# Performance work log

Hardware: AMD Instinct MI355X
Metric: run time of the kernel (lower is better)

The kernel has to match this reference:

```python
import jax, jax.numpy as jnp
import numpy as np

N = 8192          # nodes per type (MiRNA, Disease, T)
E = 500000        # edges per relation
FEAT = 256
HID = 64
OUT = 128
ITEM = 8192
SIZE = 4096
LEFT = 0
# relation order: 0:MvsD(M->D) 1:DvsM(D->M) 2:MvsT(M->T) 3:TvsM(T->M) 4:TvsD(T->D) 5:DvsT(D->T)


def graph_conv(x, W, b, src, dst, n_src, n_dst):
    outdeg = jax.ops.segment_sum(jnp.ones(src.shape, x.dtype), src, num_segments=n_src)
    xs = (x * (jnp.maximum(outdeg, 1.0) ** -0.5)[:, None]) @ W
    agg = jax.ops.segment_sum(xs[src], dst, num_segments=n_dst)
    indeg = jax.ops.segment_sum(jnp.ones(dst.shape, x.dtype), dst, num_segments=n_dst)
    return agg * (jnp.maximum(indeg, 1.0) ** -0.5)[:, None] + b


def hetero_layer(hM, hD, hT, W, b, edges):
    srcs = [hM, hD, hM, hT, hT, hD]
    outs = [graph_conv(srcs[i], W[i], b[i], edges[i, 0], edges[i, 1], N, N) for i in range(6)]
    # aggregate='sum' per destination type
    newM = outs[1] + outs[3]
    newD = outs[0] + outs[4]
    newT = outs[2] + outs[5]
    return newM, newD, newT


def setup_inputs() -> dict:
    key = jax.random.key(0)
    ks = jax.random.split(key, 24)

    def glorot(k, shape):
        lim = np.sqrt(6.0 / (shape[-2] + shape[-1]))
        return jax.random.uniform(k, shape, jnp.float32, -lim, lim)

    inp = {
        'hM': jax.random.normal(ks[0], (N, FEAT), jnp.float32),
        'hD': jax.random.normal(ks[1], (N, FEAT), jnp.float32),
        'hT': jax.random.normal(ks[2], (N, FEAT), jnp.float32),
        'W1': glorot(ks[3], (6, FEAT, HID)), 'b1': jnp.zeros((6, HID), jnp.float32),
        'W2': glorot(ks[4], (6, HID, HID)), 'b2': jnp.zeros((6, HID), jnp.float32),
        'W3': glorot(ks[5], (6, HID, OUT)), 'b3': jnp.zeros((6, OUT), jnp.float32),
        'Adj': (jax.random.uniform(ks[6], (SIZE, ITEM)) < 0.05).astype(jnp.float32),
        'f1_w': glorot(ks[7], (ITEM + OUT, 256)), 'f1_b': jnp.zeros((256,), jnp.float32),
        'f2_w': glorot(ks[8], (256, 512)), 'f2_b': jnp.zeros((512,), jnp.float32),
        'f3_w': glorot(ks[9], (512, 1024)), 'f3_b': jnp.zeros((1024,), jnp.float32),
        'f4_w': glorot(ks[10], (1024, ITEM)), 'f4_b': jnp.zeros((ITEM,), jnp.float32),
        'edges': jax.random.randint(ks[11], (6, 2, E), 0, N, dtype=jnp.int32),
        'size': SIZE,
        'leftIndex': LEFT,
    }
    return inp


def reference(hM, hD, hT, W1, b1, W2, b2, W3, b3, Adj,
              f1_w, f1_b, f2_w, f2_b, f3_w, f3_b, f4_w, f4_b,
              edges, size, leftIndex):
    hM1, hD1, hT1 = hetero_layer(hM, hD, hT, W1, b1, edges)
    hM2, hD2, hT2 = hetero_layer(hM1, hD1, hT1, W2, b2, edges)
    hM3, hD3, hT3 = hetero_layer(hM2, hD2, hT2, W3, b3, edges)
    # torch.nn.functional.normalize(p=1, dim=1)
    mirna = hM3 / jnp.maximum(jnp.sum(jnp.abs(hM3), axis=1, keepdims=True), 1e-12)
    fake_embeding = mirna[leftIndex:leftIndex + size]
    M = jnp.concatenate([Adj, fake_embeding], axis=1)
    x = jax.nn.relu(M @ f1_w + f1_b)
    x = jax.nn.relu(x @ f2_w + f2_b)
    x = jax.nn.relu(x @ f3_w + f3_b)
    x = jax.nn.sigmoid(x @ f4_w + f4_b)
    return fake_embeding, x
```

## Files before the change

kernel.cpp:

```cpp
#include <hip/hip_runtime.h>
#include <hip/hip_bf16.h>
#include <cstdint>
#include <cstddef>
#include <type_traits>

#define NN 8192
#define NTYPE 6
#define BPT 32

typedef __attribute__((ext_vector_type(8))) short bf16x8;
typedef __attribute__((ext_vector_type(4))) float f32x4;
typedef __attribute__((ext_vector_type(4))) unsigned short u16x4;
typedef __attribute__((ext_vector_type(8))) unsigned short u16x8;

#define GLOAD16(g, l)                                                        \
  __builtin_amdgcn_global_load_lds(                                          \
      (const __attribute__((address_space(1))) void*)(g),                    \
      (__attribute__((address_space(3))) void*)(l), 16, 0, 0)

static __device__ __forceinline__ unsigned short f2bf(float f) {
  union { float f; unsigned u; } x; x.f = f;
  unsigned u = x.u + 0x7fffu + ((x.u >> 16) & 1u);
  return (unsigned short)(u >> 16);
}
static __device__ __forceinline__ float bf2f(unsigned short u) {
  union { unsigned u32; float f; } x; x.u32 = (unsigned)u << 16; return x.f;
}

__global__ __launch_bounds__(256) void hist_degree(
    const int* __restrict__ edges, int* __restrict__ partial, int E) {
  const int b = blockIdx.x, t = blockIdx.y, role = blockIdx.z;
  __shared__ int h[NN];
  for (int i = threadIdx.x; i < NN; i += 256) h[i] = 0;
  __syncthreads();
  const int* ids = edges + ((size_t)t * 2 + role) * E;
  int ch = (E + BPT - 1) / BPT;
  int beg = b * ch, end = (beg + ch < E) ? beg + ch : E;
  for (int i = beg + threadIdx.x; i < end; i += 256)
    atomicAdd(&h[__builtin_nontemporal_load(ids + i)], 1);
  __syncthreads();
  int* dst = partial + ((size_t)((role * NTYPE + t) * BPT + b)) * NN;
  for (int i = threadIdx.x; i < NN; i += 256) dst[i] = h[i];
}

__global__ __launch_bounds__(256) void reduce_deg(
    const int* __restrict__ partial, float* __restrict__ inv_out,
    float* __restrict__ inv_in, int* __restrict__ incnt) {
  int i = blockIdx.x * 256 + threadIdx.x;
  if (i >= NTYPE * NN) return;
  int t = i >> 13, n = i & (NN - 1);
  const int* ps = partial + ((size_t)(t * BPT)) * NN + n;
  const int* pd = partial + ((size_t)((NTYPE + t) * BPT)) * NN + n;
  int so = 0, sd = 0;
#pragma unroll 8
  for (int b = 0; b < BPT; ++b) { so += ps[(size_t)b * NN]; sd += pd[(size_t)b * NN]; }
  inv_out[i] = rsqrtf(fmaxf((float)so, 1.0f));
  inv_in[i]  = rsqrtf(fmaxf((float)sd, 1.0f));
  incnt[i]   = sd;
}

__global__ void scan_rows(const int* __restrict__ incnt, int* __restrict__ row_start) {
  int t = blockIdx.x;
  int i = threadIdx.x;
  const int* c = incnt + t * NN;
  int v[8], s = 0;
#pragma unroll
  for (int j = 0; j < 8; ++j) { v[j] = c[i * 8 + j]; s += v[j]; }
  __shared__ int p[1024];
  p[i] = s;
  __syncthreads();
  for (int d = 1; d < 1024; d <<= 1) {
    int x = (i >= d) ? p[i - d] : 0;
    __syncthreads();
    p[i] += x;
    __syncthreads();
  }
  int run = p[i] - s;
  int* rs = row_start + t * (NN + 1);
#pragma unroll
  for (int j = 0; j < 8; ++j) { rs[i * 8 + j] = run; run += v[j]; }
  if (i == 1023) rs[NN] = run;
}

__global__ __launch_bounds__(256) void slice_offsets(
    const int* __restrict__ partial, const int* __restrict__ row_start,
    int* __restrict__ soff) {
  int i = blockIdx.x * 256 + threadIdx.x;
  if (i >= NTYPE * NN) return;
  int t = i >> 13, d = i & (NN - 1);
  const int* pd = partial + ((size_t)((NTYPE + t) * BPT)) * NN + d;
  int run = row_start[t * (NN + 1) + d];
  int* o = soff + ((size_t)t * BPT) * NN + d;
#pragma unroll 8
  for (int s = 0; s < BPT; ++s) { o[(size_t)s * NN] = run; run += pd[(size_t)s * NN]; }
}

__global__ __launch_bounds__(256) void scatter_v2(
    const int* __restrict__ edges, const int* __restrict__ soff,
    int* __restrict__ csr, int E) {
  int t = blockIdx.x;
  if (t >= NTYPE) return;
  int s = blockIdx.y;
  __shared__ int cur[NN];
  const int* o = soff + ((size_t)(t * BPT + s)) * NN;
  for (int i = threadIdx.x; i < NN; i += 256) cur[i] = o[i];
  __syncthreads();
  int ch = (E + BPT - 1) / BPT;
  int beg = s * ch, end = (beg + ch < E) ? beg + ch : E;
  const int* eb = edges + (size_t)t * 2 * E;
  int* out = csr + (size_t)t * E;
  for (int i = beg + threadIdx.x; i < end; i += 256) {
    int src = __builtin_nontemporal_load(eb + i);
    int dst = __builtin_nontemporal_load(eb + E + i);
    int pos = atomicAdd(&cur[dst], 1);
    out[pos] = src;
  }
}

__global__ __launch_bounds__(256) void gemm64xs(
    const float* __restrict__ p0, const float* __restrict__ p1,
    const float* __restrict__ p2, int lda,
    const float* __restrict__ WL, const float* __restrict__ inv_out,
    unsigned short* __restrict__ xs6, int F, int H, int tpack) {
  const int t = (tpack >> (4 * blockIdx.z)) & 15;
  const int srcc[6] = {0, 1, 0, 2, 2, 1};
  const float* A = (srcc[t] == 0) ? p0 : (srcc[t] == 1) ? p1 : p2;
  const float* B = WL + (size_t)t * F * H;
  const float* rscale = inv_out + t * NN;
  unsigned short* out = xs6 + (size_t)t * NN * H;

  __shared__ float As[16][68];
  __shared__ float Bs[16][68];
  int tid = threadIdx.x;
  int n0 = blockIdx.x * 64, m0 = blockIdx.y * 64;
  int ar = tid >> 2, ac = (tid & 3) * 4;
  int br = tid >> 4, bc = (tid & 15) * 4;
  int tx = tid & 15, ty = tid >> 4;
  float acc[4][4] = {};
  for (int k0 = 0; k0 < F; k0 += 16) {
    float4 av = *(const float4*)(A + (size_t)(m0 + ar) * lda + k0 + ac);
    As[ac + 0][ar] = av.x; As[ac + 1][ar] = av.y;
    As[ac + 2][ar] = av.z; As[ac + 3][ar] = av.w;
    *(float4*)&Bs[br][bc] = *(const float4*)(B + (size_t)(k0 + br) * H + n0 + bc);
    __syncthreads();
#pragma unroll
    for (int kk = 0; kk < 16; ++kk) {
      float4 a = *(const float4*)&As[kk][ty * 4];
      float4 b = *(const float4*)&Bs[kk][tx * 4];
      float aa[4] = {a.x, a.y, a.z, a.w};
      float bb[4] = {b.x, b.y, b.z, b.w};
#pragma unroll
      for (int i = 0; i < 4; ++i)
#pragma unroll
        for (int j = 0; j < 4; ++j) acc[i][j] += aa[i] * bb[j];
    }
    __syncthreads();
  }
#pragma unroll
  for (int i = 0; i < 4; ++i) {
    int r = m0 + ty * 4 + i;
    float sc = rscale[r];
    union { unsigned short us[4]; short4 v; } pk;
#pragma unroll
    for (int j = 0; j < 4; ++j) pk.us[j] = f2bf(acc[i][j] * sc);
    *(short4*)&out[(size_t)r * H + n0 + tx * 4] = pk.v;
  }
}

template <int H>
__global__ __launch_bounds__(256) void aggregate3(
    const unsigned short* __restrict__ xs6, const int* __restrict__ csr,
    const int* __restrict__ row_start, const float* __restrict__ inv_in,
    const float* __restrict__ bL, float* __restrict__ feat_out, int E, int cpack) {
  constexpr int VE = H / 16;
  const int c = (cpack >> (8 * blockIdx.y)) & 0xff;
  const int taT[3] = {1, 0, 2}, tbT[3] = {3, 4, 5};
  int wave = threadIdx.x >> 6, lane = threadIdx.x & 63;
  int slot = lane >> 4, colg = lane & 15;
  int d = blockIdx.x * 4 + wave;

  float out[VE];
#pragma unroll
  for (int v = 0; v < VE; ++v) out[v] = 0.f;

#pragma unroll
  for (int half = 0; half < 2; ++half) {
    int t = half ? tbT[c] : taT[c];
    const unsigned short* xs = xs6 + (size_t)t * NN * H;
    const int* cs = csr + (size_t)t * E;
    const int* rs = row_start + t * (NN + 1);
    int b = rs[d], e = rs[d + 1];
    float a[VE];
#pragma unroll
    for (int v = 0; v < VE; ++v) a[v] = 0.f;
    for (int j0 = b; j0 < e; j0 += 64) {
      int myj = j0 + lane;
      int idxv = (myj < e) ? cs[myj] : 0;
      int cnt = e - j0; if (cnt > 64) cnt = 64;
      int g = 0;
      for (; (g + 1) * 4 <= cnt; ++g) {
        int is = __shfl(idxv, g * 4 + slot);
        const unsigned short* xr = xs + (size_t)is * H + colg * VE;
        if constexpr (VE == 4) {
          u16x4 x = *(const u16x4*)xr;
#pragma unroll
          for (int v = 0; v < 4; ++v) a[v] += bf2f(x[v]);
        } else {
          u16x8 x = *(const u16x8*)xr;
#pragma unroll
          for (int v = 0; v < 8; ++v) a[v] += bf2f(x[v]);
        }
      }
      int done = g * 4;
      if (done < cnt) {
        int gi = done + slot;
        int is = __shfl(idxv, gi < cnt ? gi : 0);
        float wt = (gi < cnt) ? 1.0f : 0.0f;
        const unsigned short* xr = xs + (size_t)is * H + colg * VE;
        if constexpr (VE == 4) {
          u16x4 x = *(const u16x4*)xr;
#pragma unroll
          for (int v = 0; v < 4; ++v) a[v] += wt * bf2f(x[v]);
        } else {
          u16x8 x = *(const u16x8*)xr;
#pragma unroll
          for (int v = 0; v < 8; ++v) a[v] += wt * bf2f(x[v]);
        }
      }
    }
    float sc = inv_in[t * NN + d];
#pragma unroll
    for (int v = 0; v < VE; ++v) out[v] += a[v] * sc;
  }
#pragma unroll
  for (int v = 0; v < VE; ++v) {
    out[v] += __shfl_xor(out[v], 16);
    out[v] += __shfl_xor(out[v], 32);
  }
  if (lane < 16) {
    int ta = taT[c], tb = tbT[c];
    float* o = feat_out + (size_t)c * NN * 128 + (size_t)d * H + colg * VE;
    const float* ba = bL + ta * H + colg * VE;
    const float* bb = bL + tb * H + colg * VE;
    float4 w0 = make_float4(out[0] + ba[0] + bb[0], out[1] + ba[1] + bb[1],
                            out[2] + ba[2] + bb[2], out[3] + ba[3] + bb[3]);
    *(float4*)o = w0;
    if constexpr (VE == 8) {
      float4 w1 = make_float4(out[4] + ba[4] + bb[4], out[5] + ba[5] + bb[5],
                              out[6] + ba[6] + bb[6], out[7] + ba[7] + bb[7]);
      *(float4*)(o + 4) = w1;
    }
  }
}

__global__ __launch_bounds__(256) void l1norm_fake(
    const float* __restrict__ hM3, const int* __restrict__ leftIndex,
    float* __restrict__ fake) {
  int wave = threadIdx.x >> 6, lane = threadIdx.x & 63;
  int r = blockIdx.x * 4 + wave;
  int row = leftIndex[0] + r;
  const float* x = hM3 + (size_t)row * 128;
  float a = x[lane], b = x[64 + lane];
  float s = fabsf(a) + fabsf(b);
#pragma unroll
  for (int d = 1; d < 64; d <<= 1) s += __shfl_xor(s, d);
  float inv = 1.0f / fmaxf(s, 1e-12f);
  fake[(size_t)r * 128 + lane]      = a * inv;
  fake[(size_t)r * 128 + 64 + lane] = b * inv;
}

__global__ __launch_bounds__(256) void castT4(
    const float* __restrict__ i0, unsigned short* __restrict__ o0,
    const float* __restrict__ i1, unsigned short* __restrict__ o1,
    const float* __restrict__ i2, unsigned short* __restrict__ o2,
    const float* __restrict__ i3, unsigned short* __restrict__ o3) {
  const int nb0 = (8320 / 32) * (256 / 32);
  const int nb1 = (256 / 32) * (512 / 32);
  const int nb2 = (512 / 32) * (1024 / 32);
  int b = blockIdx.x;
  const float* in; unsigned short* out; int K, N;
  if (b < nb0) { in = i0; out = o0; K = 8320; N = 256; }
  else if ((b -= nb0) < nb1) { in = i1; out = o1; K = 256; N = 512; }
  else if ((b -= nb1) < nb2) { in = i2; out = o2; K = 512; N = 1024; }
  else { b -= nb2; in = i3; out = o3; K = 1024; N = 8192; }
  int nx = N / 32;
  int n0 = (b % nx) * 32, k0 = (b / nx) * 32;

  __shared__ float t[32][33];
  int tx = threadIdx.x & 31, ty = threadIdx.x >> 5;
#pragma unroll
  for (int i = 0; i < 32; i += 8)
    t[ty + i][tx] = in[(size_t)(k0 + ty + i) * N + n0 + tx];
  __syncthreads();
#pragma unroll
  for (int i = 0; i < 32; i += 8)
    out[(size_t)(n0 + ty + i) * K + k0 + tx] = f2bf(t[tx][ty + i]);
}

template <int ASRC, int ACT>
__global__ __launch_bounds__(256) void mfma_gemm(
    const unsigned short* __restrict__ Abf, int lda,
    const float* __restrict__ A1, const float* __restrict__ A2,
    int K1, int lda1, int lda2,
    const unsigned short* __restrict__ Bt, int ldb,
    const float* __restrict__ bias,
    void* __restrict__ outp, int ldo, int K, int kchunk, int pstride) {
  __shared__ unsigned short As[128 * 32];
  __shared__ unsigned short Bs[128 * 32];
  const int tid = threadIdx.x;
  const int n0 = blockIdx.x * 128, m0 = blockIdx.y * 128;
  const int wave = tid >> 6, lane = tid & 63;
  const int lq = lane >> 4, lr = lane & 15;
  const int wm = wave >> 1, wn = wave & 1;
  const int kbeg = blockIdx.z * kchunk;
  const int kend = (kbeg + kchunk < K) ? (kbeg + kchunk) : K;

  f32x4 acc[4][4] = {};

  const int G0 = tid, G1 = tid + 256;
  const int r0 = G0 >> 2, c0 = ((G0 & 3) - (r0 >> 1)) & 3;
  const int r1 = G1 >> 2, c1 = ((G1 & 3) - (r1 >> 1)) & 3;
  const int wbase0 = (tid & ~63) * 8;
  const int wbase1 = wbase0 + 256 * 8;

  for (int k0 = kbeg; k0 < kend; k0 += 32) {
    GLOAD16(Bt + (size_t)(n0 + r0) * ldb + k0 + c0 * 8, &Bs[wbase0]);
    GLOAD16(Bt + (size_t)(n0 + r1) * ldb + k0 + c1 * 8, &Bs[wbase1]);
    if (ASRC == 0) {
      GLOAD16(Abf + (size_t)(m0 + r0) * lda + k0 + c0 * 8, &As[wbase0]);
      GLOAD16(Abf + (size_t)(m0 + r1) * lda + k0 + c1 * 8, &As[wbase1]);
    } else {
#pragma unroll
      for (int q = 0; q < 2; ++q) {
        int r = q ? r1 : r0, c = q ? c1 : c0, G = q ? G1 : G0;
        int kk = k0 + c * 8;
        const float* src = (kk < K1) ? (A1 + (size_t)(m0 + r) * lda1 + kk)
                                     : (A2 + (size_t)(m0 + r) * lda2 + (kk - K1));
        float4 u = *(const float4*)src;
        float4 v = *(const float4*)(src + 4);
        union { unsigned short us[8]; bf16x8 v8; } pk;
        pk.us[0] = f2bf(u.x); pk.us[1] = f2bf(u.y);
        pk.us[2] = f2bf(u.z); pk.us[3] = f2bf(u.w);
        pk.us[4] = f2bf(v.x); pk.us[5] = f2bf(v.y);
        pk.us[6] = f2bf(v.z); pk.us[7] = f2bf(v.w);
        *(bf16x8*)&As[G * 8] = pk.v8;
      }
    }
    __syncthreads();

    const int cs = (lq + (lr >> 1)) & 3;
    const int rA = wm * 64 + lr, rB = wn * 64 + lr;
    bf16x8 af[4], bfr[4];
#pragma unroll
    for (int m = 0; m < 4; ++m)
      af[m] = *(const bf16x8*)&As[(((rA + m * 16) << 2) + cs) << 3];
#pragma unroll
    for (int n = 0; n < 4; ++n)
      bfr[n] = *(const bf16x8*)&Bs[(((rB + n * 16) << 2) + cs) << 3];
#pragma unroll
    for (int m = 0; m < 4; ++m)
#pragma unroll
      for (int n = 0; n < 4; ++n)
        acc[m][n] = __builtin_amdgcn_mfma_f32_16x16x32_bf16(af[m], bfr[n], acc[m][n], 0, 0, 0);
    __syncthreads();
  }

  const int rowb = m0 + wm * 64 + lq * 4;
  const int colb = n0 + wn * 64 + lr;
  float* pout = (ACT == 0) ? ((float*)outp + (size_t)blockIdx.z * pstride) : (float*)outp;
#pragma unroll
  for (int n = 0; n < 4; ++n) {
    int c = colb + n * 16;
    float bv = (ACT == 0) ? 0.0f : bias[c];
#pragma unroll
    for (int m = 0; m < 4; ++m) {
      int r = rowb + m * 16;
#pragma unroll
      for (int j = 0; j < 4; ++j) {
        float v = acc[m][n][j] + bv;
        if (ACT == 0) {
          pout[(size_t)(r + j) * ldo + c] = v;
        } else {
          v = fmaxf(v, 0.0f);
          ((unsigned short*)outp)[(size_t)(r + j) * ldo + c] = f2bf(v);
        }
      }
    }
  }
}

__global__ __launch_bounds__(512, 1) void gemm256sig(
    const unsigned short* __restrict__ A, int lda,
    const unsigned short* __restrict__ Bt, int ldb,
    const float* __restrict__ bias,
    float* __restrict__ out, int ldo) {
  __shared__ unsigned short sA[2][8192];
  __shared__ unsigned short sB[2][8192];
  const int tid = threadIdx.x;
  const int wave = tid >> 6, lane = tid & 63;
  const int lq = lane >> 4, lr = lane & 15;
  const int wm = wave >> 2, wn = wave & 3;
  const int bid = blockIdx.x;
  const int xcd = bid & 7, kb = bid >> 3;
  const int n0 = (xcd * 4 + (kb & 3)) * 256;
  const int m0 = (kb >> 2) * 256;

  f32x4 acc[8][4] = {};

  const int ra0 = tid >> 2, ca0 = tid & 3;
  const int ra1 = ra0 + 128, ca1 = ca0;
  const int sl0 = (ra0 << 2) + ((ca0 + (ra0 >> 1)) & 3);
  const int sl1 = (ra1 << 2) + ((ca1 + (ra1 >> 1)) & 3);

  u16x8 gA0, gA1, gB0, gB1;
  auto g_issue = [&](int h) {
    int kk = h * 32;
    gA0 = *(const u16x8*)(A  + (size_t)(m0 + ra0) * lda + kk + ca0 * 8);
    gA1 = *(const u16x8*)(A  + (size_t)(m0 + ra1) * lda + kk + ca1 * 8);
    gB0 = *(const u16x8*)(Bt + (size_t)(n0 + ra0) * ldb + kk + ca0 * 8);
    gB1 = *(const u16x8*)(Bt + (size_t)(n0 + ra1) * ldb + kk + ca1 * 8);
  };
  auto l_write = [&](int buf) {
    *(u16x8*)&sA[buf][sl0 * 8] = gA0;
    *(u16x8*)&sA[buf][sl1 * 8] = gA1;
    *(u16x8*)&sB[buf][sl0 * 8] = gB0;
    *(u16x8*)&sB[buf][sl1 * 8] = gB1;
  };

  g_issue(0);
  l_write(0);
  g_issue(1);
  __syncthreads();

#pragma unroll 1
  for (int h = 0; h < 32; ++h) {
    const int cur = h & 1, nxt = cur ^ 1;
    const unsigned short* pa = &sA[cur][0];
    const unsigned short* pb = &sB[cur][0];
    bf16x8 afv[8], bfv[4];
#pragma unroll
    for (int n = 0; n < 4; ++n) {
      int r = wn * 64 + n * 16 + lr;
      bfv[n] = *(const bf16x8*)&pb[(size_t)(((r << 2) + ((lq + (r >> 1)) & 3)) << 3)];
    }
#pragma unroll
    for (int m = 0; m < 8; ++m) {
      int r = wm * 128 + m * 16 + lr;
      afv[m] = *(const bf16x8*)&pa[(size_t)(((r << 2) + ((lq + (r >> 1)) & 3)) << 3)];
    }
    if (h + 1 < 32) l_write(nxt);
    if (h + 2 < 32) g_issue(h + 2);
    __builtin_amdgcn_s_setprio(1);
#pragma unroll
    for (int m = 0; m < 8; ++m)
#pragma unroll
      for (int n = 0; n < 4; ++n)
        acc[m][n] = __builtin_amdgcn_mfma_f32_16x16x32_bf16(afv[m], bfv[n], acc[m][n], 0, 0, 0);
    __builtin_amdgcn_s_setprio(0);
    __syncthreads();
  }

  float* lw = (wave < 4) ? ((float*)&sA[0][0] + wave * 2048)
                         : ((float*)&sB[0][0] + (wave - 4) * 2048);
  const int rowb = m0 + wm * 128;
  const int colb = n0 + wn * 64;
  float bv[4];
#pragma unroll
  for (int n = 0; n < 4; ++n) bv[n] = bias[colb + n * 16 + lr];
#pragma unroll
  for (int m = 0; m < 8; ++m) {
#pragma unroll
    for (int n = 0; n < 4; ++n)
#pragma unroll
      for (int j = 0; j < 4; ++j) {
        float v = acc[m][n][j] + bv[n];
        v = 1.0f / (1.0f + __expf(-v));
        lw[(lq * 4 + j) * 68 + n * 16 + lr] = v;
      }
    asm volatile("s_waitcnt lgkmcnt(0)" ::: "memory");
#pragma unroll
    for (int i = 0; i < 4; ++i) {
      int chunk = i * 64 + lane;
      int rr = chunk >> 4, cg = chunk & 15;
      f32x4 val = *(f32x4*)&lw[rr * 68 + cg * 4];
      __builtin_nontemporal_store(
          val, (f32x4*)(out + (size_t)(rowb + m * 16 + rr) * ldo + colb + cg * 4));
    }
    asm volatile("s_waitcnt lgkmcnt(0)" ::: "memory");
  }
}

__global__ __launch_bounds__(256) void reduceK(
    const float* __restrict__ part, const float* __restrict__ bias,
    unsigned short* __restrict__ out, int total, int N, int nsplit, int pstride) {
  int idx = blockIdx.x * 256 + threadIdx.x;
  int base = idx * 4;
  if (base >= total) return;
  float4 s = *(const float4*)(part + base);
  for (int z = 1; z < nsplit; ++z) {
    float4 p = *(const float4*)(part + (size_t)z * pstride + base);
    s.x += p.x; s.y += p.y; s.z += p.z; s.w += p.w;
  }
  float4 bv = *(const float4*)(bias + (base & (N - 1)));
  union { unsigned short us[4]; short4 v; } pk;
  pk.us[0] = f2bf(fmaxf(s.x + bv.x, 0.0f));
  pk.us[1] = f2bf(fmaxf(s.y + bv.y, 0.0f));
  pk.us[2] = f2bf(fmaxf(s.z + bv.z, 0.0f));
  pk.us[3] = f2bf(fmaxf(s.w + bv.w, 0.0f));
  *(short4*)&out[base] = pk.v;
}

extern "C" void kernel_launch(void* const* d_in, const int* in_sizes, int n_in,
                              void* d_out, int out_size, void* d_ws, size_t ws_size,
                              hipStream_t stream) {
  const float* hM  = (const float*)d_in[0];
  const float* hD  = (const float*)d_in[1];
  const float* hT  = (const float*)d_in[2];
  const float* W1  = (const float*)d_in[3];
  const float* b1  = (const float*)d_in[4];
  const float* W2  = (const float*)d_in[5];
  const float* b2  = (const float*)d_in[6];
  const float* W3  = (const float*)d_in[7];
  const float* b3  = (const float*)d_in[8];
  const float* Adj = (const float*)d_in[9];
  const float* f1w = (const float*)d_in[10];
  const float* f1b = (const float*)d_in[11];
  const float* f2w = (const float*)d_in[12];
  const float* f2b = (const float*)d_in[13];
  const float* f3w = (const float*)d_in[14];
  const float* f3b = (const float*)d_in[15];
  const float* f4w = (const float*)d_in[16];
  const float* f4b = (const float*)d_in[17];
  const int* edges = (const int*)d_in[18];
  const int* leftIndex = (const int*)d_in[20];
  const int E = in_sizes[18] / 12;
  (void)ws_size; (void)n_in; (void)out_size;

  char* w = (char*)d_ws;
  size_t off = 0;
  auto alloc = [&](size_t bytes) {
    void* p = w + off;
    off = (off + bytes + 255) & ~(size_t)255;
    return p;
  };
  int*   row_start = (int*)  alloc((size_t)NTYPE * (NN + 1) * 4);
  int*   incnt     = (int*)  alloc((size_t)NTYPE * NN * 4);
  float* inv_out   = (float*)alloc((size_t)NTYPE * NN * 4);
  float* inv_in    = (float*)alloc((size_t)NTYPE * NN * 4);
  float* featA     = (float*)alloc((size_t)3 * NN * 128 * 4);
  size_t ubase = off;
  int*            csr   = (int*)           alloc((size_t)NTYPE * E * 4);
  unsigned short* xs6   = (unsigned short*)alloc((size_t)NTYPE * NN * 128 * 2);
  float*          featB = (float*)         alloc((size_t)3 * NN * 128 * 4);
  int* deg_part = (int*)csr;
  int* soff     = (int*)featB;
  size_t moff = ubase;
  auto malloc2 = [&](size_t bytes) {
    void* p = w + moff;
    moff = (moff + bytes + 255) & ~(size_t)255;
    return p;
  };
  unsigned short* w1t = (unsigned short*)malloc2((size_t)256 * 8320 * 2);
  unsigned short* w2t = (unsigned short*)malloc2((size_t)512 * 256 * 2);
  unsigned short* w3t = (unsigned short*)malloc2((size_t)1024 * 512 * 2);
  unsigned short* w4t = (unsigned short*)malloc2((size_t)8192 * 1024 * 2);
  unsigned short* x1b = (unsigned short*)malloc2((size_t)4096 * 256 * 2);
  unsigned short* x2b = (unsigned short*)malloc2((size_t)4096 * 512 * 2);
  unsigned short* x3b = (unsigned short*)malloc2((size_t)4096 * 1024 * 2);
  float*          x1p = (float*)malloc2((size_t)8 * 4096 * 256 * 4);

  hist_degree<<<dim3(BPT, NTYPE, 2), 256, 0, stream>>>(edges, deg_part, E);
  reduce_deg<<<(NTYPE * NN + 255) / 256, 256, 0, stream>>>(deg_part, inv_out, inv_in, incnt);
  scan_rows<<<NTYPE, 1024, 0, stream>>>(incnt, row_start);
  slice_offsets<<<(NTYPE * NN + 255) / 256, 256, 0, stream>>>(deg_part, row_start, soff);
  scatter_v2<<<dim3(8, BPT), 256, 0, stream>>>(edges, soff, csr, E);

  const size_t comp = (size_t)NN * 128;
  gemm64xs<<<dim3(1, NN / 64, 6), 256, 0, stream>>>(
      hM, hD, hT, 256, W1, inv_out, xs6, 256, 64, 0x543210);
  aggregate3<64><<<dim3(NN / 4, 3), 256, 0, stream>>>(
      xs6, csr, row_start, inv_in, b1, featA, E, 0x020100);
  gemm64xs<<<dim3(1, NN / 64, 4), 256, 0, stream>>>(
      featA, featA + comp, featA + 2 * comp, 64, W2, inv_out, xs6, 64, 64, 0x5420);
  aggregate3<64><<<dim3(NN / 4, 2), 256, 0, stream>>>(
      xs6, csr, row_start, inv_in, b2, featB, E, 0x0201);
  gemm64xs<<<dim3(2, NN / 64, 2), 256, 0, stream>>>(
      featB, featB + comp, featB + 2 * comp, 64, W3, inv_out, xs6, 64, 128, 0x31);
  aggregate3<128><<<dim3(NN / 4, 1), 256, 0, stream>>>(
      xs6, csr, row_start, inv_in, b3, featA, E, 0x00);

  float* fake = (float*)d_out;
  float* outx = (float*)d_out + (size_t)4096 * 128;
  l1norm_fake<<<4096 / 4, 256, 0, stream>>>(featA, leftIndex, fake);

  const int ncast = (8320 / 32) * (256 / 32) + (256 / 32) * (512 / 32) +
                    (512 / 32) * (1024 / 32) + (8192 / 32) * (1024 / 32);
  castT4<<<ncast, 256, 0, stream>>>(f1w, w1t, f2w, w2t, f3w, w3t, f4w, w4t);

  mfma_gemm<1, 0><<<dim3(256 / 128, 4096 / 128, 8), 256, 0, stream>>>(
      nullptr, 0, Adj, fake, 8192, 8192, 128, w1t, 8320, nullptr,
      x1p, 256, 8320, 1056, 4096 * 256);
  reduceK<<<(4096 * 256 / 4 + 255) / 256, 256, 0, stream>>>(
      x1p, f1b, x1b, 4096 * 256, 256, 8, 4096 * 256);
  mfma_gemm<0, 1><<<dim3(512 / 128, 4096 / 128), 256, 0, stream>>>(
      x1b, 256, nullptr, nullptr, 0, 0, 0, w2t, 256, f2b, x2b, 512, 256, 256, 0);
  mfma_gemm<0, 1><<<dim3(1024 / 128, 4096 / 128), 256, 0, stream>>>(
      x2b, 512, nullptr, nullptr, 0, 0, 0, w3t, 512, f3b, x3b, 1024, 512, 512, 0);
  gemm256sig<<<512, 512, 0, stream>>>(x3b, 1024, w4t, 1024, f4b, outx, 8192);
}
```

Before: 416.0 us.

## Fuse degree/scan/offset kernels and aggregate only the needed output rows

Merges the degree reduction, row scan and slice-offset kernels into one kernel with one 1024-thread block per relation. The last-layer aggregation now computes only the 4096 destination rows starting at leftIndex that feed the MLP, instead of all 8192. The fp32 A-operand loads in the MFMA GEMM become nontemporal loads. The fused kernel removes two launches and the incnt buffer, but it runs on only 6 blocks, so the 12 MB partial-histogram read loses parallelism.

```diff
diff --git a/kernel.cpp b/kernel.cpp
--- a/kernel.cpp
+++ b/kernel.cpp
@@ -43,34 +43,34 @@
   for (int i = threadIdx.x; i < NN; i += 256) dst[i] = h[i];
 }
 
-__global__ __launch_bounds__(256) void reduce_deg(
+__global__ __launch_bounds__(1024) void build_offsets(
     const int* __restrict__ partial, float* __restrict__ inv_out,
-    float* __restrict__ inv_in, int* __restrict__ incnt) {
-  int i = blockIdx.x * 256 + threadIdx.x;
-  if (i >= NTYPE * NN) return;
-  int t = i >> 13, n = i & (NN - 1);
-  const int* ps = partial + ((size_t)(t * BPT)) * NN + n;
-  const int* pd = partial + ((size_t)((NTYPE + t) * BPT)) * NN + n;
-  int so = 0, sd = 0;
+    float* __restrict__ inv_in, int* __restrict__ row_start,
+    int* __restrict__ soff) {
+  const int t = blockIdx.x, i = threadIdx.x;
+  const int* ps = partial + (size_t)(t * BPT) * NN;
+  const int* pd = partial + (size_t)((NTYPE + t) * BPT) * NN;
+  for (int d = i; d < NN; d += 1024) {
+    int so = 0;
 #pragma unroll 8
-  for (int b = 0; b < BPT; ++b) { so += ps[(size_t)b * NN]; sd += pd[(size_t)b * NN]; }
-  inv_out[i] = rsqrtf(fmaxf((float)so, 1.0f));
-  inv_in[i]  = rsqrtf(fmaxf((float)sd, 1.0f));
-  incnt[i]   = sd;
-}
-
-__global__ void scan_rows(const int* __restrict__ incnt, int* __restrict__ row_start) {
-  int t = blockIdx.x;
-  int i = threadIdx.x;
-  const int* c = incnt + t * NN;
+    for (int b = 0; b < BPT; ++b) so += ps[(size_t)b * NN + d];
+    inv_out[t * NN + d] = rsqrtf(fmaxf((float)so, 1.0f));
+  }
   int v[8], s = 0;
 #pragma unroll
-  for (int j = 0; j < 8; ++j) { v[j] = c[i * 8 + j]; s += v[j]; }
+  for (int j = 0; j < 8; ++j) {
+    int d = i * 8 + j;
+    int sd = 0;
+#pragma unroll 8
+    for (int b = 0; b < BPT; ++b) sd += pd[(size_t)b * NN + d];
+    v[j] = sd; s += sd;
+    inv_in[t * NN + d] = rsqrtf(fmaxf((float)sd, 1.0f));
+  }
   __shared__ int p[1024];
   p[i] = s;
   __syncthreads();
-  for (int d = 1; d < 1024; d <<= 1) {
-    int x = (i >= d) ? p[i - d] : 0;
+  for (int dd = 1; dd < 1024; dd <<= 1) {
+    int x = (i >= dd) ? p[i - dd] : 0;
     __syncthreads();
     p[i] += x;
     __syncthreads();
@@ -80,19 +80,16 @@
 #pragma unroll
   for (int j = 0; j < 8; ++j) { rs[i * 8 + j] = run; run += v[j]; }
   if (i == 1023) rs[NN] = run;
-}
-
-__global__ __launch_bounds__(256) void slice_offsets(
-    const int* __restrict__ partial, const int* __restrict__ row_start,
-    int* __restrict__ soff) {
-  int i = blockIdx.x * 256 + threadIdx.x;
-  if (i >= NTYPE * NN) return;
-  int t = i >> 13, d = i & (NN - 1);
-  const int* pd = partial + ((size_t)((NTYPE + t) * BPT)) * NN + d;
-  int run = row_start[t * (NN + 1) + d];
-  int* o = soff + ((size_t)t * BPT) * NN + d;
+  __syncthreads();
+  int* o = soff + (size_t)t * BPT * NN;
+  for (int d = i; d < NN; d += 1024) {
+    int r2 = rs[d];
 #pragma unroll 8
-  for (int s = 0; s < BPT; ++s) { o[(size_t)s * NN] = run; run += pd[(size_t)s * NN]; }
+    for (int sl = 0; sl < BPT; ++sl) {
+      o[(size_t)sl * NN + d] = r2;
+      r2 += pd[(size_t)sl * NN + d];
+    }
+  }
 }
 
 __global__ __launch_bounds__(256) void scatter_v2(
@@ -171,13 +168,15 @@
 __global__ __launch_bounds__(256) void aggregate3(
     const unsigned short* __restrict__ xs6, const int* __restrict__ csr,
     const int* __restrict__ row_start, const float* __restrict__ inv_in,
-    const float* __restrict__ bL, float* __restrict__ feat_out, int E, int cpack) {
+    const float* __restrict__ bL, float* __restrict__ feat_out, int E, int cpack,
+    const int* __restrict__ dbase) {
   constexpr int VE = H / 16;
   const int c = (cpack >> (8 * blockIdx.y)) & 0xff;
   const int taT[3] = {1, 0, 2}, tbT[3] = {3, 4, 5};
   int wave = threadIdx.x >> 6, lane = threadIdx.x & 63;
   int slot = lane >> 4, colg = lane & 15;
   int d = blockIdx.x * 4 + wave;
+  if (dbase) d += dbase[0];
 
   float out[VE];
 #pragma unroll
@@ -336,13 +335,13 @@
         int kk = k0 + c * 8;
         const float* src = (kk < K1) ? (A1 + (size_t)(m0 + r) * lda1 + kk)
                                      : (A2 + (size_t)(m0 + r) * lda2 + (kk - K1));
-        float4 u = *(const float4*)src;
-        float4 v = *(const float4*)(src + 4);
+        f32x4 u = __builtin_nontemporal_load((const f32x4*)src);
+        f32x4 vv = __builtin_nontemporal_load((const f32x4*)(src + 4));
         union { unsigned short us[8]; bf16x8 v8; } pk;
-        pk.us[0] = f2bf(u.x); pk.us[1] = f2bf(u.y);
-        pk.us[2] = f2bf(u.z); pk.us[3] = f2bf(u.w);
-        pk.us[4] = f2bf(v.x); pk.us[5] = f2bf(v.y);
-        pk.us[6] = f2bf(v.z); pk.us[7] = f2bf(v.w);
+        pk.us[0] = f2bf(u[0]); pk.us[1] = f2bf(u[1]);
+        pk.us[2] = f2bf(u[2]); pk.us[3] = f2bf(u[3]);
+        pk.us[4] = f2bf(vv[0]); pk.us[5] = f2bf(vv[1]);
+        pk.us[6] = f2bf(vv[2]); pk.us[7] = f2bf(vv[3]);
         *(bf16x8*)&As[G * 8] = pk.v8;
       }
     }
@@ -544,7 +543,6 @@
     return p;
   };
   int*   row_start = (int*)  alloc((size_t)NTYPE * (NN + 1) * 4);
-  int*   incnt     = (int*)  alloc((size_t)NTYPE * NN * 4);
   float* inv_out   = (float*)alloc((size_t)NTYPE * NN * 4);
   float* inv_in    = (float*)alloc((size_t)NTYPE * NN * 4);
   float* featA     = (float*)alloc((size_t)3 * NN * 128 * 4);
@@ -570,24 +568,22 @@
   float*          x1p = (float*)malloc2((size_t)8 * 4096 * 256 * 4);
 
   hist_degree<<<dim3(BPT, NTYPE, 2), 256, 0, stream>>>(edges, deg_part, E);
-  reduce_deg<<<(NTYPE * NN + 255) / 256, 256, 0, stream>>>(deg_part, inv_out, inv_in, incnt);
-  scan_rows<<<NTYPE, 1024, 0, stream>>>(incnt, row_start);
-  slice_offsets<<<(NTYPE * NN + 255) / 256, 256, 0, stream>>>(deg_part, row_start, soff);
+  build_offsets<<<NTYPE, 1024, 0, stream>>>(deg_part, inv_out, inv_in, row_start, soff);
   scatter_v2<<<dim3(8, BPT), 256, 0, stream>>>(edges, soff, csr, E);
 
   const size_t comp = (size_t)NN * 128;
   gemm64xs<<<dim3(1, NN / 64, 6), 256, 0, stream>>>(
       hM, hD, hT, 256, W1, inv_out, xs6, 256, 64, 0x543210);
   aggregate3<64><<<dim3(NN / 4, 3), 256, 0, stream>>>(
-      xs6, csr, row_start, inv_in, b1, featA, E, 0x020100);
+      xs6, csr, row_start, inv_in, b1, featA, E, 0x020100, nullptr);
   gemm64xs<<<dim3(1, NN / 64, 4), 256, 0, stream>>>(
       featA, featA + comp, featA + 2 * comp, 64, W2, inv_out, xs6, 64, 64, 0x5420);
   aggregate3<64><<<dim3(NN / 4, 2), 256, 0, stream>>>(
-      xs6, csr, row_start, inv_in, b2, featB, E, 0x0201);
+      xs6, csr, row_start, inv_in, b2, featB, E, 0x0201, nullptr);
   gemm64xs<<<dim3(2, NN / 64, 2), 256, 0, stream>>>(
       featB, featB + comp, featB + 2 * comp, 64, W3, inv_out, xs6, 64, 128, 0x31);
-  aggregate3<128><<<dim3(NN / 4, 1), 256, 0, stream>>>(
-      xs6, csr, row_start, inv_in, b3, featA, E, 0x00);
+  aggregate3<128><<<dim3(4096 / 4, 1), 256, 0, stream>>>(
+      xs6, csr, row_start, inv_in, b3, featA, E, 0x00, leftIndex);
 
   float* fake = (float*)d_out;
   float* outx = (float*)d_out + (size_t)4096 * 128;
```

Result: slower. 573.2 us (+37.8%).
